# Performance work log

Measured on AMD Instinct MI355X. Metric: run time of the kernel, lower is better.

Reference implementation:

```python
import jax, jax.numpy as jnp
import numpy as np

PAGE_SIZE = 16
HQ, HKV, D = 32, 8, 128   # num_q_heads, num_kv_heads, head_dim
B, S = 8, 1024            # requests, tokens per request (prefill)


def setup_inputs() -> dict:
    key = jax.random.key(0)
    ks = jax.random.split(key, 4)
    T = B * S
    q = jax.random.normal(ks[0], (T, HQ * D), jnp.float32)
    k = jax.random.normal(ks[1], (T, HKV * D), jnp.float32)
    v = jax.random.normal(ks[2], (T, HKV * D), jnp.float32)
    pages_per_seq = S // PAGE_SIZE          # 64
    num_pages = B * pages_per_seq + 64      # 576 (with slack pages)
    # random page assignment: each request owns pages_per_seq distinct pages
    perm = jax.random.permutation(ks[3], num_pages)[: B * pages_per_seq]
    page_table = perm.reshape(B, pages_per_seq).astype(jnp.int32)
    key_buf = jnp.zeros((num_pages * PAGE_SIZE, HKV, D), jnp.float32)
    value_buf = jnp.zeros((num_pages * PAGE_SIZE, HKV, D), jnp.float32)
    return {"q": q, "k": k, "v": v, "key_buf": key_buf,
            "value_buf": value_buf, "page_table": page_table}


def reference(q, k, v, key_buf, value_buf, page_table):
    Bq, P = page_table.shape
    S_ = P * PAGE_SIZE
    T = Bq * S_
    scale = 1.0 / np.sqrt(D).astype(np.float32)

    k3 = k.reshape(T, HKV, D)
    v3 = v.reshape(T, HKV, D)

    # store_kv_cache: scatter new tokens into the paged KV buffers
    # token (b, s) -> slot page_table[b, s//PAGE_SIZE]*PAGE_SIZE + s%PAGE_SIZE
    slots = (page_table[:, :, None] * PAGE_SIZE
             + jnp.arange(PAGE_SIZE, dtype=page_table.dtype)).reshape(-1)  # [T]
    kb = key_buf.at[slots].set(k3)
    vb = value_buf.at[slots].set(v3)

    # prefill attention: gather each request's KV from the paged cache
    K = kb[slots].reshape(Bq, S_, HKV, D)
    V = vb[slots].reshape(Bq, S_, HKV, D)
    Q = q.reshape(Bq, S_, HKV, HQ // HKV, D)  # GQA grouping: g = HQ//HKV

    scores = jnp.einsum('bqhgd,bkhd->bhgqk', Q, K) * scale  # [B,Hkv,g,S,S]
    causal = jnp.tril(jnp.ones((S_, S_), dtype=bool))
    scores = jnp.where(causal, scores, jnp.float32(-1e30))
    p = jax.nn.softmax(scores, axis=-1)
    out = jnp.einsum('bhgqk,bkhd->bqhgd', p, V)  # [B,S,Hkv,g,D]
    return out.reshape(T, HQ * D)
```

## Files before the change

kernel.cpp:

```cpp
#include <hip/hip_runtime.h>

typedef _Float16 f16;
typedef __attribute__((ext_vector_type(8))) _Float16 f16x8;
typedef __attribute__((ext_vector_type(4))) _Float16 f16x4;
typedef __attribute__((ext_vector_type(4))) float f32x4;

constexpr int HQ = 32, HKV = 8, D = 128, NB = 8, S = 1024;
constexpr float SCALE_LOG2E = 0.08838834764831845f * 1.4426950408889634f;

__global__ __launch_bounds__(256) void pack_kernel(const float* __restrict__ k,
                                                   const float* __restrict__ v,
                                                   f16* __restrict__ kf,
                                                   f16* __restrict__ vf) {
    __shared__ __attribute__((aligned(16))) f16 tile[64][136];
    int blk = blockIdx.x;
    int tl = blk & 15, hk = (blk >> 4) & 7, b = blk >> 7;
    int t = threadIdx.x;
    size_t cbase = ((size_t)(b * 8 + hk) * 16 + tl) * 1024;

    const float* kin = k + ((size_t)(b * S + tl * 64) * HKV + hk) * D;
#pragma unroll
    for (int i = 0; i < 8; i++) {
        int flat = t + 256 * i;
        int row = flat >> 5, c4 = flat & 31;
        float4 x = *(const float4*)(kin + (size_t)row * (HKV * D) + c4 * 4);
        *(f16x4*)&tile[row][c4 * 4] = (f16x4){ (f16)x.x,(f16)x.y,(f16)x.z,(f16)x.w };
    }
    __syncthreads();
#pragma unroll
    for (int i = 0; i < 4; i++) {
        int c_loc = t + 256 * i;
        int mb = c_loc >> 8, kb = (c_loc >> 6) & 3, lane = c_loc & 63;
        int quad = lane >> 4, lq = lane & 15;
        f16x8 o = *(const f16x8*)&tile[mb * 16 + lq][kb * 32 + quad * 8];
        *(f16x8*)(kf + (cbase + c_loc) * 8) = o;
    }
    __syncthreads();

    const float* vin = v + ((size_t)(b * S + tl * 64) * HKV + hk) * D;
#pragma unroll
    for (int i = 0; i < 8; i++) {
        int flat = t + 256 * i;
        int row = flat >> 5, c4 = flat & 31;
        float4 x = *(const float4*)(vin + (size_t)row * (HKV * D) + c4 * 4);
        *(f16x4*)&tile[row][c4 * 4] = (f16x4){ (f16)x.x,(f16)x.y,(f16)x.z,(f16)x.w };
    }
    __syncthreads();
#pragma unroll
    for (int i = 0; i < 4; i++) {
        int c_loc = t + 256 * i;
        int mi = c_loc >> 7, ks2 = (c_loc >> 6) & 1, lane = c_loc & 63;
        int quad = lane >> 4, lq = lane & 15;
        int d = mi * 16 + lq;
        f16 buf[8];
#pragma unroll
        for (int o = 0; o < 2; o++)
#pragma unroll
            for (int j = 0; j < 4; j++)
                buf[o * 4 + j] = tile[ks2 * 32 + o * 16 + quad * 4 + j][d];
        *(f16x8*)(vf + (cbase + c_loc) * 8) = *(const f16x8*)buf;
    }
}

__global__ __launch_bounds__(256, 3) void attn_kernel(
    const float* __restrict__ q, const f16* __restrict__ kf,
    const f16* __restrict__ vf, float* __restrict__ out) {

    int id = blockIdx.x;
    int xcd = id & 7;
    int slot = id >> 3;
    int gl = slot >> 5;
    int inner = slot & 31;
    int g = gl * 8 + xcd;
    int b = g >> 3, hk = g & 7;
    int hq = (hk << 2) | (inner & 3);
    int qt = 7 - (((inner >> 2) + gl) & 7);

    int t = threadIdx.x;
    int w = t >> 6, lane = t & 63, quad = lane >> 4, lq = lane & 15;
    int qwb = qt * 128 + w * 32;

    f16x8 qf[2][4];
#pragma unroll
    for (int nq = 0; nq < 2; nq++) {
        int qg = qwb + nq * 16 + lq;
        const float* qp = q + ((size_t)(b * S + qg) * HQ + hq) * D + quad * 8;
#pragma unroll
        for (int kb = 0; kb < 4; kb++) {
            float4 x = *(const float4*)(qp + kb * 32);
            float4 y = *(const float4*)(qp + kb * 32 + 4);
            qf[nq][kb] = (f16x8){
                (f16)(x.x * SCALE_LOG2E), (f16)(x.y * SCALE_LOG2E),
                (f16)(x.z * SCALE_LOG2E), (f16)(x.w * SCALE_LOG2E),
                (f16)(y.x * SCALE_LOG2E), (f16)(y.y * SCALE_LOG2E),
                (f16)(y.z * SCALE_LOG2E), (f16)(y.w * SCALE_LOG2E) };
        }
    }

    f32x4 zero4 = { 0.f, 0.f, 0.f, 0.f };
    f32x4 oacc[8][2];
#pragma unroll
    for (int mi = 0; mi < 8; mi++) { oacc[mi][0] = zero4; oacc[mi][1] = zero4; }
    float m_i[2] = { -1e30f, -1e30f };
    float l_i[2] = { 0.f, 0.f };

    const f16* kfb = kf + (size_t)(b * 8 + hk) * (S * D);
    const f16* vfb = vf + (size_t)(b * 8 + hk) * (S * D);

    int nt = qwb / 64 + 1;

    for (int kt = 0; kt < nt; kt++) {
        f32x4 sacc[4][2];
#pragma unroll
        for (int mb = 0; mb < 4; mb++) { sacc[mb][0] = zero4; sacc[mb][1] = zero4; }
        __builtin_amdgcn_s_setprio(1);
#pragma unroll
        for (int mb = 0; mb < 4; mb++) {
            const f16* ka = kfb + (size_t)(((kt * 4 + mb) * 4) * 64 + lane) * 8;
#pragma unroll
            for (int kb = 0; kb < 4; kb++) {
                f16x8 af = *(const f16x8*)(ka + kb * 512);
                sacc[mb][0] = __builtin_amdgcn_mfma_f32_16x16x32_f16(af, qf[0][kb], sacc[mb][0], 0, 0, 0);
                sacc[mb][1] = __builtin_amdgcn_mfma_f32_16x16x32_f16(af, qf[1][kb], sacc[mb][1], 0, 0, 0);
            }
        }
        __builtin_amdgcn_s_setprio(0);

        bool diag = (kt == nt - 1);
        f16x4 pf[4][2];
#pragma unroll
        for (int nq = 0; nq < 2; nq++) {
            float mt = -1e30f;
            if (diag) {
                int qg = qwb + nq * 16 + lq;
#pragma unroll
                for (int mb = 0; mb < 4; mb++)
#pragma unroll
                    for (int r4 = 0; r4 < 4; r4++) {
                        float vs = sacc[mb][nq][r4];
                        int key = kt * 64 + mb * 16 + quad * 4 + r4;
                        vs = (key <= qg) ? vs : -1e30f;
                        sacc[mb][nq][r4] = vs;
                        mt = fmaxf(mt, vs);
                    }
            } else {
#pragma unroll
                for (int mb = 0; mb < 4; mb++)
#pragma unroll
                    for (int r4 = 0; r4 < 4; r4++)
                        mt = fmaxf(mt, sacc[mb][nq][r4]);
            }
            mt = fmaxf(mt, __shfl_xor(mt, 16, 64));
            mt = fmaxf(mt, __shfl_xor(mt, 32, 64));
            float mnew = m_i[nq];
            if (!__all(mt <= mnew + 8.0f)) {
                mnew = fmaxf(mnew, mt);
                float a = exp2f(m_i[nq] - mnew);
                m_i[nq] = mnew;
                l_i[nq] *= a;
#pragma unroll
                for (int mi = 0; mi < 8; mi++) oacc[mi][nq] = oacc[mi][nq] * a;
            }
            float ls = 0.f;
#pragma unroll
            for (int mb = 0; mb < 4; mb++) {
#pragma unroll
                for (int r4 = 0; r4 < 4; r4++) {
                    float e = exp2f(sacc[mb][nq][r4] - mnew);
                    sacc[mb][nq][r4] = e;
                    ls += e;
                }
                auto lo = __builtin_amdgcn_cvt_pkrtz(sacc[mb][nq][0], sacc[mb][nq][1]);
                auto hi = __builtin_amdgcn_cvt_pkrtz(sacc[mb][nq][2], sacc[mb][nq][3]);
                pf[mb][nq] = (f16x4){ (f16)lo[0], (f16)lo[1], (f16)hi[0], (f16)hi[1] };
            }
            ls += __shfl_xor(ls, 16, 64);
            ls += __shfl_xor(ls, 32, 64);
            l_i[nq] += ls;
        }

        __builtin_amdgcn_s_setprio(1);
#pragma unroll
        for (int mi = 0; mi < 8; mi++) {
            const f16* va = vfb + (size_t)(((kt * 8 + mi) * 2) * 64 + lane) * 8;
#pragma unroll
            for (int ks2 = 0; ks2 < 2; ks2++) {
                f16x8 vv = *(const f16x8*)(va + ks2 * 512);
                f16x4 v0 = { vv[0], vv[1], vv[2], vv[3] };
                f16x4 v1 = { vv[4], vv[5], vv[6], vv[7] };
                oacc[mi][0] = __builtin_amdgcn_mfma_f32_16x16x16f16(v0, pf[ks2 * 2 + 0][0], oacc[mi][0], 0, 0, 0);
                oacc[mi][0] = __builtin_amdgcn_mfma_f32_16x16x16f16(v1, pf[ks2 * 2 + 1][0], oacc[mi][0], 0, 0, 0);
                oacc[mi][1] = __builtin_amdgcn_mfma_f32_16x16x16f16(v0, pf[ks2 * 2 + 0][1], oacc[mi][1], 0, 0, 0);
                oacc[mi][1] = __builtin_amdgcn_mfma_f32_16x16x16f16(v1, pf[ks2 * 2 + 1][1], oacc[mi][1], 0, 0, 0);
            }
        }
        __builtin_amdgcn_s_setprio(0);
    }

#pragma unroll
    for (int nq = 0; nq < 2; nq++) {
        float linv = 1.0f / l_i[nq];
        int qg = qwb + nq * 16 + lq;
        float* op = out + ((size_t)(b * S + qg) * HQ + hq) * D + quad * 4;
#pragma unroll
        for (int mi = 0; mi < 8; mi++) {
            float4 vv = { oacc[mi][nq][0] * linv, oacc[mi][nq][1] * linv,
                          oacc[mi][nq][2] * linv, oacc[mi][nq][3] * linv };
            *(float4*)(op + mi * 16) = vv;
        }
    }
}

extern "C" void kernel_launch(void* const* d_in, const int* in_sizes, int n_in,
                              void* d_out, int out_size, void* d_ws, size_t ws_size,
                              hipStream_t stream) {
    (void)in_sizes; (void)n_in; (void)out_size; (void)ws_size;
    const float* q = (const float*)d_in[0];
    const float* k = (const float*)d_in[1];
    const float* v = (const float*)d_in[2];
    float* out = (float*)d_out;

    f16* kf = (f16*)d_ws;
    f16* vf = kf + (size_t)NB * HKV * S * D;

    pack_kernel<<<1024, 256, 0, stream>>>(k, v, kf, vf);
    attn_kernel<<<NB * HQ * 8, 256, 0, stream>>>(q, kf, vf, out);
}
```

Baseline: 460.9 us.

## Stage K/V tiles through double-buffered LDS with async global_load_lds

Each K and V tile is now loaded once per block into shared memory using asynchronous global-to-LDS loads, double-buffered so the next tile's load overlaps compute on the current one. Before, all four waves read the same K/V tile straight from global memory. The loop now runs to the block-wide maximum tile count with a barrier every iteration, and waves whose causal range has ended sit idle. The 64KB of LDS forces launch bounds down from 3 to 2 blocks per CU, so occupancy falls.

Result: faster. 409.0 us (-11.3%).

```diff
diff --git a/kernel.cpp b/kernel.cpp
--- a/kernel.cpp
+++ b/kernel.cpp
@@ -7,6 +7,12 @@
 
 constexpr int HQ = 32, HKV = 8, D = 128, NB = 8, S = 1024;
 constexpr float SCALE_LOG2E = 0.08838834764831845f * 1.4426950408889634f;
+
+static __device__ __forceinline__ void gload16(const f16* g, f16* l) {
+    __builtin_amdgcn_global_load_lds(
+        (const __attribute__((address_space(1))) void*)g,
+        (__attribute__((address_space(3))) void*)l, 16, 0, 0);
+}
 
 __global__ __launch_bounds__(256) void pack_kernel(const float* __restrict__ k,
                                                    const float* __restrict__ v,
@@ -62,9 +68,12 @@
     }
 }
 
-__global__ __launch_bounds__(256, 3) void attn_kernel(
+__global__ __launch_bounds__(256, 2) void attn_kernel(
     const float* __restrict__ q, const f16* __restrict__ kf,
     const f16* __restrict__ vf, float* __restrict__ out) {
+
+    __shared__ f16 ldsK[2][64 * 128];
+    __shared__ f16 ldsV[2][64 * 128];
 
     int id = blockIdx.x;
     int xcd = id & 7;
@@ -80,6 +89,19 @@
     int w = t >> 6, lane = t & 63, quad = lane >> 4, lq = lane & 15;
     int qwb = qt * 128 + w * 32;
 
+    const f16* kfb = kf + (size_t)(b * 8 + hk) * (S * D);
+    const f16* vfb = vf + (size_t)(b * 8 + hk) * (S * D);
+
+    int nt = qwb / 64 + 1;
+    int ntmax = qt * 2 + 2;
+
+#pragma unroll
+    for (int i = 0; i < 4; i++) {
+        int sl = w * 4 + i;
+        gload16(kfb + (size_t)(sl * 64 + lane) * 8, &ldsK[0][sl * 512]);
+        gload16(vfb + (size_t)(sl * 64 + lane) * 8, &ldsV[0][sl * 512]);
+    }
+
     f16x8 qf[2][4];
 #pragma unroll
     for (int nq = 0; nq < 2; nq++) {
@@ -104,97 +126,109 @@
     float m_i[2] = { -1e30f, -1e30f };
     float l_i[2] = { 0.f, 0.f };
 
-    const f16* kfb = kf + (size_t)(b * 8 + hk) * (S * D);
-    const f16* vfb = vf + (size_t)(b * 8 + hk) * (S * D);
-
-    int nt = qwb / 64 + 1;
-
-    for (int kt = 0; kt < nt; kt++) {
-        f32x4 sacc[4][2];
-#pragma unroll
-        for (int mb = 0; mb < 4; mb++) { sacc[mb][0] = zero4; sacc[mb][1] = zero4; }
-        __builtin_amdgcn_s_setprio(1);
-#pragma unroll
-        for (int mb = 0; mb < 4; mb++) {
-            const f16* ka = kfb + (size_t)(((kt * 4 + mb) * 4) * 64 + lane) * 8;
-#pragma unroll
-            for (int kb = 0; kb < 4; kb++) {
-                f16x8 af = *(const f16x8*)(ka + kb * 512);
-                sacc[mb][0] = __builtin_amdgcn_mfma_f32_16x16x32_f16(af, qf[0][kb], sacc[mb][0], 0, 0, 0);
-                sacc[mb][1] = __builtin_amdgcn_mfma_f32_16x16x32_f16(af, qf[1][kb], sacc[mb][1], 0, 0, 0);
-            }
-        }
-        __builtin_amdgcn_s_setprio(0);
-
-        bool diag = (kt == nt - 1);
-        f16x4 pf[4][2];
-#pragma unroll
-        for (int nq = 0; nq < 2; nq++) {
-            float mt = -1e30f;
-            if (diag) {
-                int qg = qwb + nq * 16 + lq;
-#pragma unroll
-                for (int mb = 0; mb < 4; mb++)
+    __syncthreads();
+
+    int cur = 0;
+    for (int kt = 0; kt < ntmax; kt++) {
+        if (kt + 1 < ntmax) {
+            const f16* kn = kfb + (size_t)(kt + 1) * (64 * 128);
+            const f16* vn = vfb + (size_t)(kt + 1) * (64 * 128);
+#pragma unroll
+            for (int i = 0; i < 4; i++) {
+                int sl = w * 4 + i;
+                gload16(kn + (size_t)(sl * 64 + lane) * 8, &ldsK[cur ^ 1][sl * 512]);
+                gload16(vn + (size_t)(sl * 64 + lane) * 8, &ldsV[cur ^ 1][sl * 512]);
+            }
+        }
+
+        if (kt < nt) {
+            f32x4 sacc[4][2];
+#pragma unroll
+            for (int mb = 0; mb < 4; mb++) { sacc[mb][0] = zero4; sacc[mb][1] = zero4; }
+            __builtin_amdgcn_s_setprio(1);
+#pragma unroll
+            for (int mb = 0; mb < 4; mb++) {
+#pragma unroll
+                for (int kb = 0; kb < 4; kb++) {
+                    f16x8 af = *(const f16x8*)&ldsK[cur][((mb * 4 + kb) * 64 + lane) * 8];
+                    sacc[mb][0] = __builtin_amdgcn_mfma_f32_16x16x32_f16(af, qf[0][kb], sacc[mb][0], 0, 0, 0);
+                    sacc[mb][1] = __builtin_amdgcn_mfma_f32_16x16x32_f16(af, qf[1][kb], sacc[mb][1], 0, 0, 0);
+                }
+            }
+            __builtin_amdgcn_s_setprio(0);
+
+            bool diag = (kt == nt - 1);
+            f16x4 pf[4][2];
+#pragma unroll
+            for (int nq = 0; nq < 2; nq++) {
+                float mt = -1e30f;
+                if (diag) {
+                    int qg = qwb + nq * 16 + lq;
+#pragma unroll
+                    for (int mb = 0; mb < 4; mb++)
+#pragma unroll
+                        for (int r4 = 0; r4 < 4; r4++) {
+                            float vs = sacc[mb][nq][r4];
+                            int key = kt * 64 + mb * 16 + quad * 4 + r4;
+                            vs = (key <= qg) ? vs : -1e30f;
+                            sacc[mb][nq][r4] = vs;
+                            mt = fmaxf(mt, vs);
+                        }
+                } else {
+#pragma unroll
+                    for (int mb = 0; mb < 4; mb++)
+#pragma unroll
+                        for (int r4 = 0; r4 < 4; r4++)
+                            mt = fmaxf(mt, sacc[mb][nq][r4]);
+                }
+                mt = fmaxf(mt, __shfl_xor(mt, 16, 64));
+                mt = fmaxf(mt, __shfl_xor(mt, 32, 64));
+                float mnew = m_i[nq];
+                if (!__all(mt <= mnew + 8.0f)) {
+                    mnew = fmaxf(mnew, mt);
+                    float a = exp2f(m_i[nq] - mnew);
+                    m_i[nq] = mnew;
+                    l_i[nq] *= a;
+#pragma unroll
+                    for (int mi = 0; mi < 8; mi++) oacc[mi][nq] = oacc[mi][nq] * a;
+                }
+                float ls = 0.f;
+#pragma unroll
+                for (int mb = 0; mb < 4; mb++) {
 #pragma unroll
                     for (int r4 = 0; r4 < 4; r4++) {
-                        float vs = sacc[mb][nq][r4];
-                        int key = kt * 64 + mb * 16 + quad * 4 + r4;
-                        vs = (key <= qg) ? vs : -1e30f;
-                        sacc[mb][nq][r4] = vs;
-                        mt = fmaxf(mt, vs);
+                        float e = exp2f(sacc[mb][nq][r4] - mnew);
+                        sacc[mb][nq][r4] = e;
+                        ls += e;
                     }
-            } else {
-#pragma unroll
-                for (int mb = 0; mb < 4; mb++)
-#pragma unroll
-                    for (int r4 = 0; r4 < 4; r4++)
-                        mt = fmaxf(mt, sacc[mb][nq][r4]);
-            }
-            mt = fmaxf(mt, __shfl_xor(mt, 16, 64));
-            mt = fmaxf(mt, __shfl_xor(mt, 32, 64));
-            float mnew = m_i[nq];
-            if (!__all(mt <= mnew + 8.0f)) {
-                mnew = fmaxf(mnew, mt);
-                float a = exp2f(m_i[nq] - mnew);
-                m_i[nq] = mnew;
-                l_i[nq] *= a;
-#pragma unroll
-                for (int mi = 0; mi < 8; mi++) oacc[mi][nq] = oacc[mi][nq] * a;
-            }
-            float ls = 0.f;
-#pragma unroll
-            for (int mb = 0; mb < 4; mb++) {
-#pragma unroll
-                for (int r4 = 0; r4 < 4; r4++) {
-                    float e = exp2f(sacc[mb][nq][r4] - mnew);
-                    sacc[mb][nq][r4] = e;
-                    ls += e;
-                }
-                auto lo = __builtin_amdgcn_cvt_pkrtz(sacc[mb][nq][0], sacc[mb][nq][1]);
-                auto hi = __builtin_amdgcn_cvt_pkrtz(sacc[mb][nq][2], sacc[mb][nq][3]);
-                pf[mb][nq] = (f16x4){ (f16)lo[0], (f16)lo[1], (f16)hi[0], (f16)hi[1] };
-            }
-            ls += __shfl_xor(ls, 16, 64);
-            ls += __shfl_xor(ls, 32, 64);
-            l_i[nq] += ls;
-        }
-
-        __builtin_amdgcn_s_setprio(1);
-#pragma unroll
-        for (int mi = 0; mi < 8; mi++) {
-            const f16* va = vfb + (size_t)(((kt * 8 + mi) * 2) * 64 + lane) * 8;
-#pragma unroll
-            for (int ks2 = 0; ks2 < 2; ks2++) {
-                f16x8 vv = *(const f16x8*)(va + ks2 * 512);
-                f16x4 v0 = { vv[0], vv[1], vv[2], vv[3] };
-                f16x4 v1 = { vv[4], vv[5], vv[6], vv[7] };
-                oacc[mi][0] = __builtin_amdgcn_mfma_f32_16x16x16f16(v0, pf[ks2 * 2 + 0][0], oacc[mi][0], 0, 0, 0);
-                oacc[mi][0] = __builtin_amdgcn_mfma_f32_16x16x16f16(v1, pf[ks2 * 2 + 1][0], oacc[mi][0], 0, 0, 0);
-                oacc[mi][1] = __builtin_amdgcn_mfma_f32_16x16x16f16(v0, pf[ks2 * 2 + 0][1], oacc[mi][1], 0, 0, 0);
-                oacc[mi][1] = __builtin_amdgcn_mfma_f32_16x16x16f16(v1, pf[ks2 * 2 + 1][1], oacc[mi][1], 0, 0, 0);
-            }
-        }
-        __builtin_amdgcn_s_setprio(0);
+                    auto lo = __builtin_amdgcn_cvt_pkrtz(sacc[mb][nq][0], sacc[mb][nq][1]);
+                    auto hi = __builtin_amdgcn_cvt_pkrtz(sacc[mb][nq][2], sacc[mb][nq][3]);
+                    pf[mb][nq] = (f16x4){ (f16)lo[0], (f16)lo[1], (f16)hi[0], (f16)hi[1] };
+                }
+                ls += __shfl_xor(ls, 16, 64);
+                ls += __shfl_xor(ls, 32, 64);
+                l_i[nq] += ls;
+            }
+
+            __builtin_amdgcn_s_setprio(1);
+#pragma unroll
+            for (int mi = 0; mi < 8; mi++) {
+#pragma unroll
+                for (int ks2 = 0; ks2 < 2; ks2++) {
+                    f16x8 vv = *(const f16x8*)&ldsV[cur][((mi * 2 + ks2) * 64 + lane) * 8];
+                    f16x4 v0 = { vv[0], vv[1], vv[2], vv[3] };
+                    f16x4 v1 = { vv[4], vv[5], vv[6], vv[7] };
+                    oacc[mi][0] = __builtin_amdgcn_mfma_f32_16x16x16f16(v0, pf[ks2 * 2 + 0][0], oacc[mi][0], 0, 0, 0);
+                    oacc[mi][0] = __builtin_amdgcn_mfma_f32_16x16x16f16(v1, pf[ks2 * 2 + 1][0], oacc[mi][0], 0, 0, 0);
+                    oacc[mi][1] = __builtin_amdgcn_mfma_f32_16x16x16f16(v0, pf[ks2 * 2 + 0][1], oacc[mi][1], 0, 0, 0);
+                    oacc[mi][1] = __builtin_amdgcn_mfma_f32_16x16x16f16(v1, pf[ks2 * 2 + 1][1], oacc[mi][1], 0, 0, 0);
+                }
+            }
+            __builtin_amdgcn_s_setprio(0);
+        }
+
+        __syncthreads();
+        cur ^= 1;
     }
 
 #pragma unroll
```
